# Kernel tuning notes

Hardware: AMD Instinct MI355X
Metric: run time of the kernel (lower is better)

## Reference

```python
import jax, jax.numpy as jnp
import numpy as np
from jax import lax

B, C, H, W = 8, 256, 128, 128
NH = 8
HD = C // NH
EPS = 1e-5


def setup_inputs() -> dict:
    key = jax.random.key(0)
    ks = jax.random.split(key, 6)
    x = jax.random.normal(ks[0], (B, C, H, W), dtype=jnp.float32)
    dw_weight = jax.random.normal(ks[1], (C, 1, 3, 3), dtype=jnp.float32) * 0.1
    off_weight = jax.random.normal(ks[2], (NH * 2, C), dtype=jnp.float32) * 0.05
    off_bias = jnp.zeros((NH * 2,), dtype=jnp.float32)
    v_weight = jax.random.normal(ks[3], (C, C), dtype=jnp.float32) * (1.0 / np.sqrt(C))
    o_weight = jax.random.normal(ks[4], (C, C), dtype=jnp.float32) * (1.0 / np.sqrt(C))
    gamma = jnp.ones((C,), dtype=jnp.float32)
    beta = jnp.zeros((C,), dtype=jnp.float32)
    return {"x": x, "dw_weight": dw_weight, "off_weight": off_weight, "off_bias": off_bias,
            "v_weight": v_weight, "o_weight": o_weight, "gamma": gamma, "beta": beta}


def reference(x, dw_weight, off_weight, off_bias, v_weight, o_weight, gamma, beta):
    b, c, h, w = x.shape
    # --- offset branch: depthwise 3x3 + pointwise 1x1 ---
    hdw = lax.conv_general_dilated(x, dw_weight, (1, 1), 'SAME',
                                   feature_group_count=c,
                                   dimension_numbers=('NCHW', 'OIHW', 'NCHW'))
    offsets = jnp.einsum('bchw,oc->bohw', hdw, off_weight) + off_bias[None, :, None, None]
    offsets = jnp.tanh(offsets) * 0.5                      # (B, 2*NH, H, W)
    offsets = offsets.reshape(b, NH, 2, h, w)
    dy, dx = offsets[:, :, 0], offsets[:, :, 1]            # (B, NH, H, W)

    # --- value projection, split into heads ---
    V = jnp.einsum('bchw,oc->bohw', x, v_weight).reshape(b, NH, HD, h, w)

    # --- deformable bilinear sampling (grid_sample, align_corners=True, border pad) ---
    gy = jnp.linspace(-1.0, 1.0, h, dtype=x.dtype)[None, None, :, None]
    gx = jnp.linspace(-1.0, 1.0, w, dtype=x.dtype)[None, None, None, :]
    sx = jnp.clip(gx + dx, -1.0, 1.0)                      # (B, NH, H, W)
    sy = jnp.clip(gy + dy, -1.0, 1.0)
    ix = (sx + 1.0) * 0.5 * (w - 1)                        # unnormalized coords
    iy = (sy + 1.0) * 0.5 * (h - 1)
    x0f = jnp.floor(ix); y0f = jnp.floor(iy)
    wx = ix - x0f; wy = iy - y0f
    x0 = jnp.clip(x0f.astype(jnp.int32), 0, w - 1)
    x1 = jnp.clip(x0f.astype(jnp.int32) + 1, 0, w - 1)
    y0 = jnp.clip(y0f.astype(jnp.int32), 0, h - 1)
    y1 = jnp.clip(y0f.astype(jnp.int32) + 1, 0, h - 1)

    Vf = V.reshape(b, NH, HD, h * w)

    def gather(yi, xi):
        idx = (yi * w + xi).reshape(b, NH, 1, h * w)
        return jnp.take_along_axis(Vf, idx, axis=3)        # (B, NH, HD, H*W)

    wx_ = wx.reshape(b, NH, 1, h * w); wy_ = wy.reshape(b, NH, 1, h * w)
    sampled = (gather(y0, x0) * (1 - wx_) * (1 - wy_)
               + gather(y0, x1) * wx_ * (1 - wy_)
               + gather(y1, x0) * (1 - wx_) * wy_
               + gather(y1, x1) * wx_ * wy_)
    out = sampled.reshape(b, c, h, w)

    # --- output projection + GroupNorm(NH groups) + residual ---
    out = jnp.einsum('bchw,oc->bohw', out, o_weight)
    g = out.reshape(b, NH, HD * h * w)
    mu = jnp.mean(g, axis=-1, keepdims=True)
    var = jnp.mean(jnp.square(g - mu), axis=-1, keepdims=True)
    g = (g - mu) * lax.rsqrt(var + EPS)
    out = g.reshape(b, c, h, w) * gamma[None, :, None, None] + beta[None, :, None, None]
    return x + out
```

## Files before the change

### kernel.cpp

```cpp
#include <hip/hip_runtime.h>
#include <hip/hip_bf16.h>

#define B_ 8
#define C_ 256
#define H_ 128
#define W_ 128
#define HW_ 16384
#define CHW_ (C_ * HW_)
#define NH_ 8
#define HD_ 32
#define NTOT (B_ * CHW_)

typedef short short8 __attribute__((ext_vector_type(8)));
typedef float f32x4 __attribute__((ext_vector_type(4)));

__global__ __launch_bounds__(256) void wconv_kernel(const float* __restrict__ vw,
                                                    const float* __restrict__ ow,
                                                    __hip_bfloat16* __restrict__ wvb,
                                                    __hip_bfloat16* __restrict__ wob) {
    int i = blockIdx.x * 256 + threadIdx.x;
    wvb[i] = __float2bfloat16(vw[i]);
    wob[i] = __float2bfloat16(ow[i]);
}

__global__ __launch_bounds__(256) void xt_kernel(const float* __restrict__ x,
                                                 __hip_bfloat16* __restrict__ xT) {
    __shared__ float tile[64][68];
    int t = threadIdx.x;
    int p0 = blockIdx.x * 64, c0 = blockIdx.y * 64, b = blockIdx.z;
    const float* xb = x + ((size_t)b * C_ + c0) * HW_ + p0;
#pragma unroll
    for (int l = 0; l < 4; ++l) {
        int idx = t + 256 * l;
        int row = idx >> 4, cf = idx & 15;
        float4 v = *(const float4*)&xb[(size_t)row * HW_ + cf * 4];
        *(float4*)&tile[row][cf * 4] = v;
    }
    __syncthreads();
    __hip_bfloat16* op = xT + ((size_t)b * HW_ + p0) * C_ + c0;
#pragma unroll
    for (int l = 0; l < 2; ++l) {
        int idx = t + 256 * l;
        int p = idx & 63, oct = idx >> 6;
        __hip_bfloat16 arr[8];
#pragma unroll
        for (int j = 0; j < 8; ++j) arr[j] = __float2bfloat16(tile[oct * 8 + j][p]);
        *(int4*)(op + (size_t)p * C_ + oct * 8) = *(int4*)arr;
    }
}

__global__ __launch_bounds__(256) void fused_offset_kernel(const float* __restrict__ x,
                                                           const float* __restrict__ dww,
                                                           const float* __restrict__ offw,
                                                           float* __restrict__ partials) {
    __shared__ float xt[4][10][136];
    __shared__ float wT[32][16];
    __shared__ float wd[32][9];
    int t = threadIdx.x;
    int rt = blockIdx.x, cg = blockIdx.y, b = blockIdx.z;
    int h0 = rt * 8, c0 = cg * 32;
    for (int i = t; i < 512; i += 256) { int o = i >> 5, c = i & 31; wT[c][o] = offw[o * 256 + c0 + c]; }
    for (int i = t; i < 288; i += 256) { wd[i / 9][i % 9] = dww[(c0 + i / 9) * 9 + i % 9]; }
    const float* xb = x + ((size_t)b * C_ + c0) * HW_;
    int col = t & 127;
    int sb = (t >> 7) * 4;
    float acc[4][16] = {};
    for (int cc0 = 0; cc0 < 32; cc0 += 4) {
        __syncthreads();
#pragma unroll
        for (int l = 0; l < 5; ++l) {
            int idx = t + 256 * l;
            int pr = idx >> 5, c4 = idx & 31;
            int cc = pr / 10, r = pr - cc * 10;
            int gh = h0 - 1 + r;
            float4 v = make_float4(0.f, 0.f, 0.f, 0.f);
            if (gh >= 0 && gh < H_)
                v = *(const float4*)&xb[(size_t)(cc0 + cc) * HW_ + gh * W_ + c4 * 4];
            *(float4*)&xt[cc][r][4 + c4 * 4] = v;
        }
        if (t < 80) { int pr = t >> 1, side = t & 1; xt[pr / 10][pr % 10][side ? 132 : 3] = 0.f; }
        __syncthreads();
#pragma unroll
        for (int cc = 0; cc < 4; ++cc) {
            float win[6][3];
#pragma unroll
            for (int rr = 0; rr < 6; ++rr)
#pragma unroll
                for (int kk = 0; kk < 3; ++kk)
                    win[rr][kk] = xt[cc][sb + rr][col + 3 + kk];
            float w9[9];
#pragma unroll
            for (int k9 = 0; k9 < 9; ++k9) w9[k9] = wd[cc0 + cc][k9];
#pragma unroll
            for (int j = 0; j < 4; ++j) {
                float s = 0.f;
#pragma unroll
                for (int ky = 0; ky < 3; ++ky)
#pragma unroll
                    for (int kx = 0; kx < 3; ++kx)
                        s += win[j + ky][kx] * w9[ky * 3 + kx];
#pragma unroll
                for (int o = 0; o < 16; ++o) acc[j][o] += s * wT[cc0 + cc][o];
            }
        }
    }
    float* pb = partials + (size_t)(cg * 8 + b) * 16 * HW_;
#pragma unroll
    for (int o = 0; o < 16; ++o)
#pragma unroll
        for (int j = 0; j < 4; ++j)
            pb[(size_t)o * HW_ + (h0 + sb + j) * W_ + col] = acc[j][o];
}

__global__ __launch_bounds__(256) void offreduce_kernel(const float* __restrict__ partials,
                                                        const float* __restrict__ offb,
                                                        float* __restrict__ off_buf) {
    int i = blockIdx.x * 256 + threadIdx.x;
    float s = 0.f;
#pragma unroll
    for (int cg = 0; cg < 8; ++cg) s += partials[(size_t)cg * 2097152 + i];
    int o = (i >> 14) & 15;
    off_buf[i] = tanhf(s + offb[o]) * 0.5f;
}

template<bool TRANS, bool STATS>
__global__ __launch_bounds__(256, 4) void mfma_gemm(const __hip_bfloat16* __restrict__ Wb,
                                                    const __hip_bfloat16* __restrict__ Xt,
                                                    void* __restrict__ Y,
                                                    float* __restrict__ stats) {
    __shared__ __align__(16) short As[128 * 32];
    __shared__ __align__(16) short Bs[128 * 32];
    int t = threadIdx.x;
    int wave = t >> 6, lane = t & 63;
    int quad = lane >> 4, l16 = lane & 15;
    int b = blockIdx.z;
    int n0 = blockIdx.x * 128, m0 = blockIdx.y * 128;
    const short* Wp = (const short*)Wb + (size_t)m0 * 256;
    const short* Xp = (const short*)Xt + ((size_t)b * HW_ + n0) * 256;

    int i0 = t, i1 = t + 256;
    int r0 = i0 >> 2, r1 = i1 >> 2;
    int ss0 = (i0 & 3) ^ ((r0 >> 1) & 3);
    int ss1 = (i1 & 3) ^ ((r1 >> 1) & 3);

    f32x4 acc[2][8];
#pragma unroll
    for (int mt = 0; mt < 2; ++mt)
#pragma unroll
        for (int nt = 0; nt < 8; ++nt) acc[mt][nt] = (f32x4){0.f, 0.f, 0.f, 0.f};

    for (int kk = 0; kk < 8; ++kk) {
        int ko = kk * 32;
        __builtin_amdgcn_global_load_lds(Wp + (size_t)r0 * 256 + ko + ss0 * 8, &As[i0 * 8], 16, 0, 0);
        __builtin_amdgcn_global_load_lds(Wp + (size_t)r1 * 256 + ko + ss1 * 8, &As[i1 * 8], 16, 0, 0);
        __builtin_amdgcn_global_load_lds(Xp + (size_t)r0 * 256 + ko + ss0 * 8, &Bs[i0 * 8], 16, 0, 0);
        __builtin_amdgcn_global_load_lds(Xp + (size_t)r1 * 256 + ko + ss1 * 8, &Bs[i1 * 8], 16, 0, 0);
        __syncthreads();
        short8 af[2], bf[8];
#pragma unroll
        for (int mt = 0; mt < 2; ++mt) {
            int r = wave * 32 + mt * 16 + l16;
            int sl = quad ^ ((r >> 1) & 3);
            af[mt] = *(const short8*)&As[r * 32 + sl * 8];
        }
#pragma unroll
        for (int nt = 0; nt < 8; ++nt) {
            int r = nt * 16 + l16;
            int sl = quad ^ ((r >> 1) & 3);
            bf[nt] = *(const short8*)&Bs[r * 32 + sl * 8];
        }
#pragma unroll
        for (int mt = 0; mt < 2; ++mt)
#pragma unroll
            for (int nt = 0; nt < 8; ++nt)
                acc[mt][nt] = __builtin_amdgcn_mfma_f32_16x16x32_bf16(af[mt], bf[nt], acc[mt][nt], 0, 0, 0);
        __syncthreads();
    }

    if constexpr (TRANS) {
        __hip_bfloat16* Yb = (__hip_bfloat16*)Y + (size_t)b * CHW_;
#pragma unroll
        for (int mt = 0; mt < 2; ++mt)
#pragma unroll
            for (int nt = 0; nt < 8; ++nt) {
                int m = m0 + wave * 32 + mt * 16 + quad * 4;
                int n = n0 + nt * 16 + l16;
                __hip_bfloat16 arr[4];
#pragma unroll
                for (int r = 0; r < 4; ++r) arr[r] = __float2bfloat16(acc[mt][nt][r]);
                *(int2*)((__hip_bfloat16*)Yb + (size_t)n * C_ + m) = *(int2*)arr;
            }
    } else {
        float* Yb = (float*)Y + (size_t)b * CHW_;
#pragma unroll
        for (int mt = 0; mt < 2; ++mt)
#pragma unroll
            for (int nt = 0; nt < 8; ++nt)
#pragma unroll
                for (int r = 0; r < 4; ++r) {
                    int m = m0 + wave * 32 + mt * 16 + quad * 4 + r;
                    int n = n0 + nt * 16 + l16;
                    Yb[(size_t)m * HW_ + n] = acc[mt][nt][r];
                }
    }
    if constexpr (STATS) {
        float s1 = 0.f, s2 = 0.f;
#pragma unroll
        for (int mt = 0; mt < 2; ++mt)
#pragma unroll
            for (int nt = 0; nt < 8; ++nt)
#pragma unroll
                for (int r = 0; r < 4; ++r) {
                    float v = acc[mt][nt][r];
                    s1 += v;
                    s2 += v * v;
                }
#pragma unroll
        for (int o = 32; o; o >>= 1) {
            s1 += __shfl_down(s1, o);
            s2 += __shfl_down(s2, o);
        }
        if (lane == 0) {
            int grp = b * NH_ + (m0 >> 5) + wave;
            atomicAdd(&stats[grp * 2 + 0], s1);
            atomicAdd(&stats[grp * 2 + 1], s2);
        }
    }
}

__global__ __launch_bounds__(256) void sample_kernel(const __hip_bfloat16* __restrict__ VT,
                                                     const float* __restrict__ off,
                                                     __hip_bfloat16* __restrict__ sT) {
    int t = threadIdx.x;
    int chunk = t & 3;
    int g = t >> 2;
    int head = g & 7;
    int p = blockIdx.x * 8 + (g >> 3);
    int b = blockIdx.z;
    int h = p >> 7, w = p & 127;
    const float* ob = off + ((size_t)b * 16 + head * 2) * HW_ + p;
    float dy = ob[0], dx = ob[HW_];
    float gy = h * (2.0f / 127.0f) - 1.0f;
    float gx = w * (2.0f / 127.0f) - 1.0f;
    float sx = fminf(fmaxf(gx + dx, -1.0f), 1.0f);
    float sy = fminf(fmaxf(gy + dy, -1.0f), 1.0f);
    float ix = (sx + 1.0f) * 0.5f * 127.0f;
    float iy = (sy + 1.0f) * 0.5f * 127.0f;
    float x0f = floorf(ix), y0f = floorf(iy);
    float wx = ix - x0f, wy = iy - y0f;
    int x0 = min(max((int)x0f, 0), 127);
    int x1 = min((int)x0f + 1, 127);
    int y0 = min(max((int)y0f, 0), 127);
    int y1 = min((int)y0f + 1, 127);
    float w00 = (1.f - wx) * (1.f - wy), w01 = wx * (1.f - wy);
    float w10 = (1.f - wx) * wy, w11 = wx * wy;
    const short* Vb = (const short*)VT + (size_t)b * CHW_ + head * 32 + chunk * 8;
    short8 v00 = *(const short8*)(Vb + (size_t)(y0 * W_ + x0) * C_);
    short8 v01 = *(const short8*)(Vb + (size_t)(y0 * W_ + x1) * C_);
    short8 v10 = *(const short8*)(Vb + (size_t)(y1 * W_ + x0) * C_);
    short8 v11 = *(const short8*)(Vb + (size_t)(y1 * W_ + x1) * C_);
    __hip_bfloat16 arr[8];
#pragma unroll
    for (int j = 0; j < 8; ++j) {
        float f = __bfloat162float(((const __hip_bfloat16*)&v00)[j]) * w00 +
                  __bfloat162float(((const __hip_bfloat16*)&v01)[j]) * w01 +
                  __bfloat162float(((const __hip_bfloat16*)&v10)[j]) * w10 +
                  __bfloat162float(((const __hip_bfloat16*)&v11)[j]) * w11;
        arr[j] = __float2bfloat16(f);
    }
    __hip_bfloat16* op = sT + ((size_t)b * HW_ + p) * C_ + head * 32 + chunk * 8;
    *(int4*)op = *(int4*)arr;
}

__global__ __launch_bounds__(256) void final_kernel(const float* __restrict__ x,
                                                    const float* __restrict__ stats,
                                                    const float* __restrict__ gamma,
                                                    const float* __restrict__ beta,
                                                    float* __restrict__ out) {
    int idx = (blockIdx.x * 256 + threadIdx.x) * 4;
    int c = (idx >> 14) & 255;
    int b = idx >> 22;
    int grp = b * NH_ + (c >> 5);
    const float invN = 1.0f / (float)(HD_ * HW_);
    float mu = stats[grp * 2 + 0] * invN;
    float var = stats[grp * 2 + 1] * invN - mu * mu;
    float r = rsqrtf(var + 1e-5f);
    float g = gamma[c], be = beta[c];
    float4 v = *(const float4*)&out[idx];
    float4 xv = *(const float4*)&x[idx];
    float4 o;
    o.x = xv.x + (v.x - mu) * r * g + be;
    o.y = xv.y + (v.y - mu) * r * g + be;
    o.z = xv.z + (v.z - mu) * r * g + be;
    o.w = xv.w + (v.w - mu) * r * g + be;
    *(float4*)&out[idx] = o;
}

extern "C" void kernel_launch(void* const* d_in, const int* in_sizes, int n_in,
                              void* d_out, int out_size, void* d_ws, size_t ws_size,
                              hipStream_t stream) {
    const float* x     = (const float*)d_in[0];
    const float* dww   = (const float*)d_in[1];
    const float* offw  = (const float*)d_in[2];
    const float* offb  = (const float*)d_in[3];
    const float* vw    = (const float*)d_in[4];
    const float* ow    = (const float*)d_in[5];
    const float* gamma = (const float*)d_in[6];
    const float* beta  = (const float*)d_in[7];
    float* out = (float*)d_out;
    float* ws_f = (float*)d_ws;

    float* partials = ws_f;
    float* off_buf  = ws_f + 16777216;
    float* stats    = ws_f + 18874368;
    __hip_bfloat16* wvb = (__hip_bfloat16*)(ws_f + 18874624);
    __hip_bfloat16* wob = wvb + 65536;
    __hip_bfloat16* xT  = (__hip_bfloat16*)(ws_f + 18940160);
    __hip_bfloat16* sT  = (__hip_bfloat16*)partials;
    __hip_bfloat16* vT  = (__hip_bfloat16*)out;

    wconv_kernel<<<256, 256, 0, stream>>>(vw, ow, wvb, wob);
    xt_kernel<<<dim3(256, 4, 8), 256, 0, stream>>>(x, xT);
    fused_offset_kernel<<<dim3(16, 8, 8), 256, 0, stream>>>(x, dww, offw, partials);
    offreduce_kernel<<<8192, 256, 0, stream>>>(partials, offb, off_buf);
    mfma_gemm<true, false><<<dim3(128, 2, 8), 256, 0, stream>>>(wvb, xT, (void*)vT, nullptr);
    sample_kernel<<<dim3(2048, 1, 8), 256, 0, stream>>>(vT, off_buf, sT);
    hipMemsetAsync(stats, 0, 128 * sizeof(float), stream);
    mfma_gemm<false, true><<<dim3(128, 2, 8), 256, 0, stream>>>(wob, sT, (void*)out, stats);
    final_kernel<<<NTOT / 1024, 256, 0, stream>>>(x, stats, gamma, beta, out);
}
```

Before: 572.1 us.

## Double-buffer GEMM LDS tiles and stage transposed bf16 output through LDS

Splits the MFMA GEMM shared memory into two buffers so the next K-slice's global-to-LDS loads are issued before computing on the current slice, cutting one barrier per iteration and hiding load latency. The transposed bf16 epilogue now writes the tile into padded LDS first and then issues coalesced 16-byte global stores, replacing scattered 8-byte stores. LDS use grows to about 34 KB per block, which may limit occupancy under the 4-blocks-per-SM launch bound.

```diff
diff --git a/kernel.cpp b/kernel.cpp
--- a/kernel.cpp
+++ b/kernel.cpp
@@ -128,8 +128,7 @@
                                                     const __hip_bfloat16* __restrict__ Xt,
                                                     void* __restrict__ Y,
                                                     float* __restrict__ stats) {
-    __shared__ __align__(16) short As[128 * 32];
-    __shared__ __align__(16) short Bs[128 * 32];
+    __shared__ __align__(16) short smem[17408];
     int t = threadIdx.x;
     int wave = t >> 6, lane = t & 63;
     int quad = lane >> 4, l16 = lane & 15;
@@ -143,31 +142,44 @@
     int ss0 = (i0 & 3) ^ ((r0 >> 1) & 3);
     int ss1 = (i1 & 3) ^ ((r1 >> 1) & 3);
 
+#define STAGE(buf, ko)                                                                                          \
+    do {                                                                                                        \
+        short* Asm_ = smem + (buf) * 4096;                                                                      \
+        short* Bsm_ = smem + 8192 + (buf) * 4096;                                                               \
+        __builtin_amdgcn_global_load_lds(Wp + (size_t)r0 * 256 + (ko) + ss0 * 8, Asm_ + i0 * 8, 16, 0, 0);      \
+        __builtin_amdgcn_global_load_lds(Wp + (size_t)r1 * 256 + (ko) + ss1 * 8, Asm_ + i1 * 8, 16, 0, 0);      \
+        __builtin_amdgcn_global_load_lds(Xp + (size_t)r0 * 256 + (ko) + ss0 * 8, Bsm_ + i0 * 8, 16, 0, 0);      \
+        __builtin_amdgcn_global_load_lds(Xp + (size_t)r1 * 256 + (ko) + ss1 * 8, Bsm_ + i1 * 8, 16, 0, 0);      \
+    } while (0)
+
     f32x4 acc[2][8];
 #pragma unroll
     for (int mt = 0; mt < 2; ++mt)
 #pragma unroll
         for (int nt = 0; nt < 8; ++nt) acc[mt][nt] = (f32x4){0.f, 0.f, 0.f, 0.f};
 
+    STAGE(0, 0);
+    __syncthreads();
+
+#pragma unroll
     for (int kk = 0; kk < 8; ++kk) {
-        int ko = kk * 32;
-        __builtin_amdgcn_global_load_lds(Wp + (size_t)r0 * 256 + ko + ss0 * 8, &As[i0 * 8], 16, 0, 0);
-        __builtin_amdgcn_global_load_lds(Wp + (size_t)r1 * 256 + ko + ss1 * 8, &As[i1 * 8], 16, 0, 0);
-        __builtin_amdgcn_global_load_lds(Xp + (size_t)r0 * 256 + ko + ss0 * 8, &Bs[i0 * 8], 16, 0, 0);
-        __builtin_amdgcn_global_load_lds(Xp + (size_t)r1 * 256 + ko + ss1 * 8, &Bs[i1 * 8], 16, 0, 0);
-        __syncthreads();
+        int cur = kk & 1;
+        if (kk < 7) STAGE(cur ^ 1, (kk + 1) * 32);
+        __builtin_amdgcn_sched_barrier(0);
+        const short* Ac = smem + cur * 4096;
+        const short* Bc = smem + 8192 + cur * 4096;
         short8 af[2], bf[8];
 #pragma unroll
         for (int mt = 0; mt < 2; ++mt) {
             int r = wave * 32 + mt * 16 + l16;
             int sl = quad ^ ((r >> 1) & 3);
-            af[mt] = *(const short8*)&As[r * 32 + sl * 8];
+            af[mt] = *(const short8*)&Ac[r * 32 + sl * 8];
         }
 #pragma unroll
         for (int nt = 0; nt < 8; ++nt) {
             int r = nt * 16 + l16;
             int sl = quad ^ ((r >> 1) & 3);
-            bf[nt] = *(const short8*)&Bs[r * 32 + sl * 8];
+            bf[nt] = *(const short8*)&Bc[r * 32 + sl * 8];
         }
 #pragma unroll
         for (int mt = 0; mt < 2; ++mt)
@@ -176,20 +188,29 @@
                 acc[mt][nt] = __builtin_amdgcn_mfma_f32_16x16x32_bf16(af[mt], bf[nt], acc[mt][nt], 0, 0, 0);
         __syncthreads();
     }
+#undef STAGE
 
     if constexpr (TRANS) {
-        __hip_bfloat16* Yb = (__hip_bfloat16*)Y + (size_t)b * CHW_;
 #pragma unroll
         for (int mt = 0; mt < 2; ++mt)
 #pragma unroll
             for (int nt = 0; nt < 8; ++nt) {
-                int m = m0 + wave * 32 + mt * 16 + quad * 4;
-                int n = n0 + nt * 16 + l16;
+                int n = nt * 16 + l16;
+                int mloc = wave * 32 + mt * 16 + quad * 4;
                 __hip_bfloat16 arr[4];
 #pragma unroll
                 for (int r = 0; r < 4; ++r) arr[r] = __float2bfloat16(acc[mt][nt][r]);
-                *(int2*)((__hip_bfloat16*)Yb + (size_t)n * C_ + m) = *(int2*)arr;
+                *(int2*)&smem[n * 136 + mloc] = *(int2*)arr;
             }
+        __syncthreads();
+        short* Yb = (short*)Y + (size_t)b * CHW_;
+#pragma unroll
+        for (int i = 0; i < 8; ++i) {
+            int id = t + 256 * i;
+            int row = id >> 4, c = id & 15;
+            int4 v = *(const int4*)&smem[row * 136 + c * 8];
+            *(int4*)(Yb + (size_t)(n0 + row) * 256 + m0 + c * 8) = v;
+        }
     } else {
         float* Yb = (float*)Y + (size_t)b * CHW_;
 #pragma unroll
```

Measured after the change: 558.3 us. -2.4%, faster.
